# Optimization experiments

Measured on AMD Instinct MI355X. Metric: run time of the kernel, lower is better.

## Reference

```python
import jax, jax.numpy as jnp
import numpy as np

H, I, B, S = 3200, 12800, 8, 1024  # InternViT-6B MLP dims


def setup_inputs() -> dict:
    key = jax.random.key(0)
    ks = jax.random.split(key, 8)
    # int8-valued activations/weights stored as int32 (harness dtype set)
    hidden_states = jax.random.randint(ks[0], (B, S, H), -127, 128, dtype=jnp.int32)
    scale = jax.random.uniform(ks[1], (B * S,), dtype=jnp.float32) * 1e-3 + 1e-5
    w1 = jax.random.randint(ks[2], (I, H), -127, 128, dtype=jnp.int32)
    w1_scale = jax.random.uniform(ks[3], (I,), dtype=jnp.float32) * 1e-3 + 1e-5
    b1 = jax.random.normal(ks[4], (I,), dtype=jnp.float32) * 0.02
    w2 = jax.random.randint(ks[5], (H, I), -127, 128, dtype=jnp.int32)
    w2_scale = jax.random.uniform(ks[6], (H,), dtype=jnp.float32) * 1e-3 + 1e-5
    b2 = jax.random.normal(ks[7], (H,), dtype=jnp.float32) * 0.02
    return {"hidden_states": hidden_states, "scale": scale, "w1": w1,
            "w1_scale": w1_scale, "b1": b1, "w2": w2, "w2_scale": w2_scale, "b2": b2}


def _w8a8_linear(x_q, x_scale, w_q, w_scale, b):
    # enough that fp32 matmul reproduces the exact integer accumulator to
    # within float32 rounding of the final sum.
    acc = jnp.matmul(x_q.astype(jnp.float32), w_q.astype(jnp.float32).T)  # [T, out]
    out = acc * x_scale[:, None] * w_scale[None, :] + b[None, :]
    return out.astype(jnp.float16)


def reference(hidden_states, scale, w1, w1_scale, b1, w2, w2_scale, b2):
    bsz, seq, hidden = hidden_states.shape
    x_q = hidden_states.reshape(-1, hidden)                 # [T, H] int8 values
    # fc1: W8A8 -> fp16 with dynamic per-token input scale
    fc1_out = _w8a8_linear(x_q, scale, w1, w1_scale, b1)    # [T, I] fp16
    # fused gelu_and_quant: exact GELU, then per-token dynamic int8 re-quant
    g = jax.nn.gelu(fc1_out.astype(jnp.float32), approximate=False)  # [T, I]
    new_scale = jnp.max(jnp.abs(g), axis=-1) / 127.0        # dynamic per-token scale
    act_q = jnp.clip(jnp.round(g / new_scale[:, None]), -127, 127)  # int8 values
    # fc2: W8A8 -> fp16
    out = _w8a8_linear(act_q, new_scale, w2, w2_scale, b2)  # [T, H] fp16
    return out
```

## Files before the change

### kernel.cpp

```cpp
#include <hip/hip_runtime.h>
#include <hip/hip_bf16.h>
#include <hip/hip_fp16.h>

#define T_DIM 8192
#define H_DIM 3200
#define I_DIM 12800

typedef int v4i __attribute__((ext_vector_type(4)));
typedef _Float16 h8 __attribute__((ext_vector_type(8)));

__device__ __forceinline__ void gload16(const void* g, void* l) {
    __builtin_amdgcn_global_load_lds(
        (const __attribute__((address_space(1))) unsigned int*)g,
        (__attribute__((address_space(3))) unsigned int*)l, 16, 0, 0);
}

__global__ __launch_bounds__(256) void repack_kernel(const int* __restrict__ src,
                                                     unsigned int* __restrict__ dst,
                                                     long n4) {
    long i = (long)blockIdx.x * blockDim.x + threadIdx.x;
    long stride = (long)gridDim.x * blockDim.x;
    for (; i < n4; i += stride) {
        int4 v = ((const int4*)src)[i];
        dst[i] = (unsigned int)((v.x & 255) | ((v.y & 255) << 8) |
                                ((v.z & 255) << 16) | ((v.w & 255) << 24));
    }
}

template <int EPI>
__global__ __launch_bounds__(256, 2) void gemm_i8(
    const signed char* __restrict__ A, long strideA,
    const signed char* __restrict__ B,
    int M, int N, int K,
    const float* __restrict__ rowscale, const float* __restrict__ colscale,
    const float* __restrict__ bias, void* __restrict__ Cout) {
    __shared__ signed char ldsA[2][128 * 64];
    __shared__ signed char ldsB[2][128 * 64];

    const int tid = threadIdx.x;
    const int lane = tid & 63;
    const int wid = tid >> 6;
    const int wr = wid >> 1, wc = wid & 1;
    const int bm = blockIdx.x, bn = blockIdx.y;

    const long Arow0 = (long)bm * 128;
    const long Bcol0 = (long)bn * 128;

    const int c0 = tid, c1 = tid + 256;
    const signed char* Ag0 = A + (Arow0 + (c0 >> 2)) * strideA + ((c0 & 3) << 4);
    const signed char* Ag1 = A + (Arow0 + (c1 >> 2)) * strideA + ((c1 & 3) << 4);
    const signed char* Bg0 = B + (Bcol0 + (c0 >> 2)) * (long)K + ((c0 & 3) << 4);
    const signed char* Bg1 = B + (Bcol0 + (c1 >> 2)) * (long)K + ((c1 & 3) << 4);

#define STAGE(buf, kt)                                   \
    {                                                    \
        long ko = (long)(kt) << 6;                       \
        gload16(Ag0 + ko, &ldsA[buf][c0 * 16]);          \
        gload16(Ag1 + ko, &ldsA[buf][c1 * 16]);          \
        gload16(Bg0 + ko, &ldsB[buf][c0 * 16]);          \
        gload16(Bg1 + ko, &ldsB[buf][c1 * 16]);          \
    }

    v4i acc[4][4] = {};

    const int nk = K >> 6;
    STAGE(0, 0);
    int cur = 0;
    const int r = lane & 15, q = lane >> 4;
    for (int kt = 0; kt < nk; ++kt) {
        __syncthreads();
        if (kt + 1 < nk) STAGE(cur ^ 1, kt + 1);
        const v4i* Al = (const v4i*)ldsA[cur];
        const v4i* Bl = (const v4i*)ldsB[cur];
        v4i a[4], b[4];
#pragma unroll
        for (int m = 0; m < 4; ++m) a[m] = Al[(wr * 64 + m * 16 + r) * 4 + q];
#pragma unroll
        for (int n = 0; n < 4; ++n) b[n] = Bl[(wc * 64 + n * 16 + r) * 4 + q];
#pragma unroll
        for (int m = 0; m < 4; ++m)
#pragma unroll
            for (int n = 0; n < 4; ++n)
                acc[m][n] = __builtin_amdgcn_mfma_i32_16x16x64_i8(a[m], b[n], acc[m][n], 0, 0, 0);
        cur ^= 1;
    }

    const int row0 = bm * 128 + wr * 64;
    const int col0 = bn * 128 + wc * 64;
    const int r4 = (lane >> 4) * 4, cl = lane & 15;
#pragma unroll
    for (int m = 0; m < 4; ++m) {
#pragma unroll
        for (int n = 0; n < 4; ++n) {
            const int col = col0 + n * 16 + cl;
            const float cs = colscale[col];
            const float bs = bias[col];
#pragma unroll
            for (int rr = 0; rr < 4; ++rr) {
                const int row = row0 + m * 16 + r4 + rr;
                float v = (float)acc[m][n][rr];
                v = __fmul_rn(v, rowscale[row]);
                v = __fmul_rn(v, cs);
                v = __fadd_rn(v, bs);
                _Float16 hh = (_Float16)v;
                if (EPI == 0) {
                    ((_Float16*)Cout)[(size_t)row * N + col] = hh;
                } else {
                    ((float*)Cout)[(size_t)row * N + col] = (float)hh;
                }
            }
        }
    }
#undef STAGE
}

__global__ __launch_bounds__(256) void gelu_quant(_Float16* __restrict__ fc1,
                                                  float* __restrict__ nscale) {
    __shared__ float gbuf[I_DIM];
    __shared__ float wmax[4];
    const int tid = threadIdx.x, lane = tid & 63, wid = tid >> 6;
    const long t = blockIdx.x;
    const h8* row = (const h8*)(fc1 + t * I_DIM);
    float lmax = 0.f;
    for (int c = tid; c < I_DIM / 8; c += 256) {
        h8 v = row[c];
#pragma unroll
        for (int j = 0; j < 8; ++j) {
            float x = (float)v[j];
            float e = erff(__fdiv_rn(x, 1.41421356237309504880f));
            float g = __fmul_rn(__fmul_rn(0.5f, x), __fadd_rn(1.0f, e));
            gbuf[c * 8 + j] = g;
            lmax = fmaxf(lmax, fabsf(g));
        }
    }
#pragma unroll
    for (int off = 32; off; off >>= 1) lmax = fmaxf(lmax, __shfl_xor(lmax, off, 64));
    if (lane == 0) wmax[wid] = lmax;
    __syncthreads();
    const float gmax = fmaxf(fmaxf(wmax[0], wmax[1]), fmaxf(wmax[2], wmax[3]));
    const float ns = gmax / 127.0f;
    if (tid == 0) nscale[t] = ns;
    unsigned long long* out = (unsigned long long*)(fc1 + t * I_DIM);
    for (int c = tid; c < I_DIM / 8; c += 256) {
        unsigned long long pk = 0;
#pragma unroll
        for (int j = 0; j < 8; ++j) {
            float qv = rintf(__fdiv_rn(gbuf[c * 8 + j], ns));
            qv = fminf(fmaxf(qv, -127.f), 127.f);
            pk |= ((unsigned long long)(unsigned char)(signed char)(int)qv) << (8 * j);
        }
        out[c] = pk;
    }
}

extern "C" void kernel_launch(void* const* d_in, const int* in_sizes, int n_in,
                              void* d_out, int out_size, void* d_ws, size_t ws_size,
                              hipStream_t stream) {
    const int* hs = (const int*)d_in[0];
    const float* scale = (const float*)d_in[1];
    const int* w1 = (const int*)d_in[2];
    const float* w1s = (const float*)d_in[3];
    const float* b1 = (const float*)d_in[4];
    const int* w2 = (const int*)d_in[5];
    const float* w2s = (const float*)d_in[6];
    const float* b2 = (const float*)d_in[7];

    char* ws = (char*)d_ws;
    signed char* xq = (signed char*)ws;
    signed char* w1q = xq + (size_t)T_DIM * H_DIM;
    signed char* w2q = w1q + (size_t)I_DIM * H_DIM;
    _Float16* fc1h = (_Float16*)(w2q + (size_t)H_DIM * I_DIM);
    const size_t fixed = (size_t)T_DIM * H_DIM + 2 * (size_t)I_DIM * H_DIM;

    int nc = 1;
    while (nc < 16) {
        size_t need = fixed + ((size_t)T_DIM / nc) * I_DIM * 2 +
                      ((size_t)T_DIM / nc) * 4 + 256;
        if (need <= ws_size) break;
        nc <<= 1;
    }
    const int chunkT = T_DIM / nc;
    float* nscale = (float*)((char*)fc1h + (size_t)chunkT * I_DIM * 2);

    repack_kernel<<<2048, 256, 0, stream>>>(hs, (unsigned int*)xq, (long)T_DIM * H_DIM / 4);
    repack_kernel<<<2048, 256, 0, stream>>>(w1, (unsigned int*)w1q, (long)I_DIM * H_DIM / 4);
    repack_kernel<<<2048, 256, 0, stream>>>(w2, (unsigned int*)w2q, (long)H_DIM * I_DIM / 4);

    for (int c = 0; c < nc; ++c) {
        const int t0 = c * chunkT;
        gemm_i8<0><<<dim3(chunkT / 128, I_DIM / 128), 256, 0, stream>>>(
            xq + (size_t)t0 * H_DIM, (long)H_DIM, w1q, chunkT, I_DIM, H_DIM,
            scale + t0, w1s, b1, (void*)fc1h);
        gelu_quant<<<chunkT, 256, 0, stream>>>(fc1h, nscale);
        gemm_i8<1><<<dim3(chunkT / 128, H_DIM / 128), 256, 0, stream>>>(
            (const signed char*)fc1h, (long)I_DIM * 2, w2q, chunkT, H_DIM, I_DIM,
            nscale, w2s, b2,
            (void*)((float*)d_out + (size_t)t0 * H_DIM));
    }
}
```

Measured before the change: 1.052 ms.

## Rewrite int8 GEMM as 256x256 eight-wave tile with four-stage swizzled LDS pipeline

Replaces the 128x128, 4-wave, double-buffered int8 MFMA GEMM with a 256x256 tile computed by 8 waves. Operands stream through a 4-slot ring of 64-wide K slices in 128KB of LDS, with an XOR swizzle on the 16-byte chunks. The K loop is split into barrier-separated phases that interleave async global-to-LDS loads with MFMA bursts raised to higher priority. The aim is more data reuse per LDS byte, better latency hiding and fewer bank conflicts. In exchange, LDS use allows only one block per CU, and the last fc2 column tile reads past the true N (masked in the epilogue).

```diff
diff --git a/kernel.cpp b/kernel.cpp
--- a/kernel.cpp
+++ b/kernel.cpp
@@ -28,90 +28,132 @@
 }
 
 template <int EPI>
-__global__ __launch_bounds__(256, 2) void gemm_i8(
+__global__ __launch_bounds__(512, 2) void gemm_i8_8ph(
     const signed char* __restrict__ A, long strideA,
-    const signed char* __restrict__ B,
-    int M, int N, int K,
+    const signed char* __restrict__ B, long strideB,
+    int Ntrue, int K, int ldc,
     const float* __restrict__ rowscale, const float* __restrict__ colscale,
     const float* __restrict__ bias, void* __restrict__ Cout) {
-    __shared__ signed char ldsA[2][128 * 64];
-    __shared__ signed char ldsB[2][128 * 64];
+    __shared__ signed char lds[131072];
+    signed char* ldsA = lds;
+    signed char* ldsB = lds + 65536;
 
     const int tid = threadIdx.x;
-    const int lane = tid & 63;
-    const int wid = tid >> 6;
-    const int wr = wid >> 1, wc = wid & 1;
+    const int lane = tid & 63, wid = tid >> 6;
+    const int wr = wid >> 2, wc = wid & 3;
     const int bm = blockIdx.x, bn = blockIdx.y;
-
-    const long Arow0 = (long)bm * 128;
-    const long Bcol0 = (long)bn * 128;
-
-    const int c0 = tid, c1 = tid + 256;
-    const signed char* Ag0 = A + (Arow0 + (c0 >> 2)) * strideA + ((c0 & 3) << 4);
-    const signed char* Ag1 = A + (Arow0 + (c1 >> 2)) * strideA + ((c1 & 3) << 4);
-    const signed char* Bg0 = B + (Bcol0 + (c0 >> 2)) * (long)K + ((c0 & 3) << 4);
-    const signed char* Bg1 = B + (Bcol0 + (c1 >> 2)) * (long)K + ((c1 & 3) << 4);
-
-#define STAGE(buf, kt)                                   \
-    {                                                    \
-        long ko = (long)(kt) << 6;                       \
-        gload16(Ag0 + ko, &ldsA[buf][c0 * 16]);          \
-        gload16(Ag1 + ko, &ldsA[buf][c1 * 16]);          \
-        gload16(Bg0 + ko, &ldsB[buf][c0 * 16]);          \
-        gload16(Bg1 + ko, &ldsB[buf][c1 * 16]);          \
-    }
-
-    v4i acc[4][4] = {};
-
-    const int nk = K >> 6;
-    STAGE(0, 0);
-    int cur = 0;
+    const long Arow0 = (long)bm * 256;
+    const long Bcol0 = (long)bn * 256;
+
+    const int c0 = tid, c1 = tid + 512;
+    const int r0 = c0 >> 2, r1 = c1 >> 2;
+    const int s0 = (((c0 & 3) ^ ((r0 >> 1) & 3)) << 4);
+    const int s1 = (((c1 & 3) ^ ((r1 >> 1) & 3)) << 4);
+    const signed char* Ag0 = A + (Arow0 + r0) * strideA + s0;
+    const signed char* Ag1 = A + (Arow0 + r1) * strideA + s1;
+    const signed char* Bg0 = B + (Bcol0 + r0) * strideB + s0;
+    const signed char* Bg1 = B + (Bcol0 + r1) * strideB + s1;
+    const int d0 = c0 * 16, d1 = c1 * 16;
+
+    const int NH = K >> 6;
+    const int nkt = K >> 7;
+
+#define STAGE_A(h)                                  \
+    {                                               \
+        const int hc_ = (h) < NH ? (h) : NH - 1;    \
+        const long ko_ = (long)hc_ << 6;            \
+        signed char* d_ = ldsA + (((h) & 3) << 14); \
+        gload16(Ag0 + ko_, d_ + d0);                \
+        gload16(Ag1 + ko_, d_ + d1);                \
+    }
+#define STAGE_B(h)                                  \
+    {                                               \
+        const int hc_ = (h) < NH ? (h) : NH - 1;    \
+        const long ko_ = (long)hc_ << 6;            \
+        signed char* d_ = ldsB + (((h) & 3) << 14); \
+        gload16(Bg0 + ko_, d_ + d0);                \
+        gload16(Bg1 + ko_, d_ + d1);                \
+    }
+
     const int r = lane & 15, q = lane >> 4;
-    for (int kt = 0; kt < nk; ++kt) {
-        __syncthreads();
-        if (kt + 1 < nk) STAGE(cur ^ 1, kt + 1);
-        const v4i* Al = (const v4i*)ldsA[cur];
-        const v4i* Bl = (const v4i*)ldsB[cur];
-        v4i a[4], b[4];
-#pragma unroll
-        for (int m = 0; m < 4; ++m) a[m] = Al[(wr * 64 + m * 16 + r) * 4 + q];
-#pragma unroll
-        for (int n = 0; n < 4; ++n) b[n] = Bl[(wc * 64 + n * 16 + r) * 4 + q];
-#pragma unroll
-        for (int m = 0; m < 4; ++m)
-#pragma unroll
-            for (int n = 0; n < 4; ++n)
-                acc[m][n] = __builtin_amdgcn_mfma_i32_16x16x64_i8(a[m], b[n], acc[m][n], 0, 0, 0);
-        cur ^= 1;
-    }
-
-    const int row0 = bm * 128 + wr * 64;
-    const int col0 = bn * 128 + wc * 64;
-    const int r4 = (lane >> 4) * 4, cl = lane & 15;
-#pragma unroll
-    for (int m = 0; m < 4; ++m) {
+    const int swz = ((q ^ ((r >> 1) & 3)) << 4);
+    const int aoff = (wr * 128 + r) * 64 + swz;
+    const int boff = (wc * 64 + r) * 64 + swz;
+
+    v4i acc[8][4] = {};
+    v4i af[4], bf[4];
+
+#define PHASE(SLOTA, SLOTB, AIDX, LOADB, ACCOFF, STAGE_STMT, GATE_STMT)     \
+    {                                                                       \
+        _Pragma("unroll") for (int i = 0; i < 4; ++i)                       \
+            af[i] = *(const v4i*)((SLOTA) + aoff + ((AIDX) + i) * 1024);    \
+        if (LOADB) {                                                        \
+            _Pragma("unroll") for (int n = 0; n < 4; ++n)                   \
+                bf[n] = *(const v4i*)((SLOTB) + boff + n * 1024);           \
+        }                                                                   \
+        STAGE_STMT;                                                         \
+        __builtin_amdgcn_s_barrier();                                       \
+        asm volatile("s_waitcnt lgkmcnt(0)");                               \
+        __builtin_amdgcn_s_setprio(1);                                      \
+        _Pragma("unroll") for (int m = 0; m < 4; ++m)                       \
+            _Pragma("unroll") for (int n = 0; n < 4; ++n)                   \
+                acc[m + (ACCOFF)][n] = __builtin_amdgcn_mfma_i32_16x16x64_i8( \
+                    af[m], bf[n], acc[m + (ACCOFF)][n], 0, 0, 0);           \
+        __builtin_amdgcn_s_setprio(0);                                      \
+        GATE_STMT;                                                          \
+        __builtin_amdgcn_s_barrier();                                       \
+    }
+
+    STAGE_B(0); STAGE_A(0); STAGE_B(1); STAGE_A(1);
+    STAGE_B(2); STAGE_A(2); STAGE_B(3);
+    asm volatile("s_waitcnt vmcnt(6)");
+    __builtin_amdgcn_s_barrier();
+
+    for (int kt = 0; kt < nkt; ++kt) {
+        const int g = kt << 1;
+        const signed char* sA0 = ldsA + ((g & 3) << 14);
+        const signed char* sB0 = ldsB + ((g & 3) << 14);
+        const signed char* sA1 = ldsA + (((g + 1) & 3) << 14);
+        const signed char* sB1 = ldsB + (((g + 1) & 3) << 14);
+        PHASE(sA0, sB0, 0, true, 0, STAGE_A(g + 3), );
+        PHASE(sA0, sB0, 4, false, 4, STAGE_B(g + 4), );
+        PHASE(sA1, sB1, 0, true, 0, STAGE_A(g + 4), );
+        PHASE(sA1, sB1, 4, false, 4, STAGE_B(g + 5),
+              asm volatile("s_waitcnt vmcnt(6)"));
+    }
+
+    const int row0 = bm * 256 + wr * 128;
+    const int col0 = bn * 256 + wc * 64;
+    const int r4 = (lane >> 4) << 2, cl = lane & 15;
+#pragma unroll
+    for (int m = 0; m < 8; ++m) {
+        const int rowb = row0 + m * 16 + r4;
+        float rs[4];
+#pragma unroll
+        for (int rr = 0; rr < 4; ++rr) rs[rr] = rowscale[rowb + rr];
 #pragma unroll
         for (int n = 0; n < 4; ++n) {
             const int col = col0 + n * 16 + cl;
-            const float cs = colscale[col];
-            const float bs = bias[col];
-#pragma unroll
-            for (int rr = 0; rr < 4; ++rr) {
-                const int row = row0 + m * 16 + r4 + rr;
-                float v = (float)acc[m][n][rr];
-                v = __fmul_rn(v, rowscale[row]);
-                v = __fmul_rn(v, cs);
-                v = __fadd_rn(v, bs);
-                _Float16 hh = (_Float16)v;
-                if (EPI == 0) {
-                    ((_Float16*)Cout)[(size_t)row * N + col] = hh;
-                } else {
-                    ((float*)Cout)[(size_t)row * N + col] = (float)hh;
+            if (col < Ntrue) {
+                const float cs = colscale[col];
+                const float bs = bias[col];
+#pragma unroll
+                for (int rr = 0; rr < 4; ++rr) {
+                    float v = (float)acc[m][n][rr];
+                    v = __fmul_rn(v, rs[rr]);
+                    v = __fmul_rn(v, cs);
+                    v = __fadd_rn(v, bs);
+                    _Float16 hh = (_Float16)v;
+                    const size_t idx = (size_t)(rowb + rr) * ldc + col;
+                    if (EPI == 0) ((_Float16*)Cout)[idx] = hh;
+                    else ((float*)Cout)[idx] = (float)hh;
                 }
             }
         }
     }
-#undef STAGE
+#undef PHASE
+#undef STAGE_A
+#undef STAGE_B
 }
 
 __global__ __launch_bounds__(256) void gelu_quant(_Float16* __restrict__ fc1,
@@ -186,14 +228,17 @@
     repack_kernel<<<2048, 256, 0, stream>>>(w1, (unsigned int*)w1q, (long)I_DIM * H_DIM / 4);
     repack_kernel<<<2048, 256, 0, stream>>>(w2, (unsigned int*)w2q, (long)H_DIM * I_DIM / 4);
 
+    const int n2tiles = (H_DIM + 255) / 256;
     for (int c = 0; c < nc; ++c) {
         const int t0 = c * chunkT;
-        gemm_i8<0><<<dim3(chunkT / 128, I_DIM / 128), 256, 0, stream>>>(
-            xq + (size_t)t0 * H_DIM, (long)H_DIM, w1q, chunkT, I_DIM, H_DIM,
+        gemm_i8_8ph<0><<<dim3(chunkT / 256, I_DIM / 256), 512, 0, stream>>>(
+            xq + (size_t)t0 * H_DIM, (long)H_DIM, w1q, (long)H_DIM,
+            I_DIM, H_DIM, I_DIM,
             scale + t0, w1s, b1, (void*)fc1h);
         gelu_quant<<<chunkT, 256, 0, stream>>>(fc1h, nscale);
-        gemm_i8<1><<<dim3(chunkT / 128, H_DIM / 128), 256, 0, stream>>>(
-            (const signed char*)fc1h, (long)I_DIM * 2, w2q, chunkT, H_DIM, I_DIM,
+        gemm_i8_8ph<1><<<dim3(chunkT / 256, n2tiles), 512, 0, stream>>>(
+            (const signed char*)fc1h, (long)I_DIM * 2, w2q, (long)I_DIM,
+            H_DIM, I_DIM, H_DIM,
             nscale, w2s, b2,
             (void*)((float*)d_out + (size_t)t0 * H_DIM));
     }
```

After: 966.1 us. -8.1%, faster.
